# Performance work log

Hardware: AMD Instinct MI355X
Metric: run time of the kernel (lower is better)

The kernel has to match this reference:

```python
import jax, jax.numpy as jnp
import numpy as np

N, E = 100000, 1600000
IN_F, HID, OUT_F, HEADS = 256, 128, 64, 1
C = HID // HEADS  # per-head channels (=128 for heads=1)
NEG_SLOPE = 0.2   # PyG GATConv default leaky_relu slope


def setup_inputs() -> dict:
    key = jax.random.key(0)
    ks = jax.random.split(key, 16)
    w = lambda k, shape, fan: (jax.random.normal(k, shape, jnp.float32) / np.float32(np.sqrt(fan)))
    return {
        "x": jax.random.normal(ks[0], (N, IN_F), jnp.float32),
        "edge_index": jax.random.randint(ks[1], (2, E), 0, N, dtype=jnp.int32),
        "W_in": w(ks[2], (IN_F, HID), IN_F),
        "b_in": jnp.zeros((HID,), jnp.float32),
        "W1": w(ks[3], (HID, HEADS * C), HID),
        "att_src1": w(ks[4], (HEADS, C), C),
        "att_dst1": w(ks[5], (HEADS, C), C),
        "bias1": jnp.zeros((C,), jnp.float32),
        "W2": w(ks[6], (HID, HEADS * C), HID),
        "att_src2": w(ks[7], (HEADS, C), C),
        "att_dst2": w(ks[8], (HEADS, C), C),
        "bias2": jnp.zeros((C,), jnp.float32),
        "W_out": w(ks[9], (HID, OUT_F), HID),
        "b_out": jnp.zeros((OUT_F,), jnp.float32),
    }


def gat_conv(h, src, dst, W, a_src, a_dst, bias):
    """PyG GATConv, concat=False: per-head attention, segment softmax over dst, mean over heads."""
    g = (h @ W).reshape(-1, HEADS, C)                      # [N,H,C]
    alpha_src = jnp.einsum("nhc,hc->nh", g, a_src)         # [N,H]
    alpha_dst = jnp.einsum("nhc,hc->nh", g, a_dst)         # [N,H]
    e = jax.nn.leaky_relu(alpha_src[src] + alpha_dst[dst], NEG_SLOPE)  # [E,H]
    m = jax.ops.segment_max(e, dst, num_segments=N)        # [N,H], -inf for empty segments
    m = jnp.where(jnp.isfinite(m), m, 0.0)
    p = jnp.exp(e - m[dst])
    s = jax.ops.segment_sum(p, dst, num_segments=N)        # [N,H]
    alpha = p / (s[dst] + 1e-16)                           # [E,H]
    msg = g[src] * alpha[..., None]                        # [E,H,C]  (dominant traffic)
    out = jax.ops.segment_sum(msg, dst, num_segments=N)    # [N,H,C]
    return out.mean(axis=1) + bias                         # concat=False -> head average


def reference(x, edge_index, W_in, b_in, W1, att_src1, att_dst1, bias1,
              W2, att_src2, att_dst2, bias2, W_out, b_out):
    src, dst = edge_index[0], edge_index[1]
    h = x @ W_in + b_in
    h = jax.nn.relu(gat_conv(h, src, dst, W1, att_src1, att_dst1, bias1))
    h = jax.nn.relu(gat_conv(h, src, dst, W2, att_src2, att_dst2, bias2))
    return h @ W_out + b_out
```

## Files before the change

### kernel.cpp

```cpp
#include <hip/hip_runtime.h>
#include <hip/hip_fp16.h>
#include <math.h>

#define NN 100000
#define EE 1600000
constexpr int IN_F = 256, HID = 128, OUT_F = 64;

#define NB 196
#define CAP 16384
#define CH 4096
#define NCHUNK 391

#define MAXE 128

typedef __bf16 bf16x8 __attribute__((ext_vector_type(8)));
typedef float  f32x4  __attribute__((ext_vector_type(4)));

__device__ __forceinline__ f32x4 mfma16(bf16x8 a, bf16x8 b, f32x4 c){
  return __builtin_amdgcn_mfma_f32_16x16x32_bf16(a, b, c, 0, 0, 0);
}

__device__ __forceinline__ void fmamix2(float& aLo, float& aHi, __half2 g2, float al){
  asm("v_fma_mix_f32 %0, %2, %3, %0 op_sel:[0,0,0] op_sel_hi:[1,0,0]\n\t"
      "v_fma_mix_f32 %1, %2, %3, %1 op_sel:[1,0,0] op_sel_hi:[1,0,0]"
      : "+v"(aLo), "+v"(aHi) : "v"(g2), "v"(al));
}

__device__ __forceinline__ float wred_max(float v){
#pragma unroll
  for (int m=1; m<64; m<<=1) v = fmaxf(v, __shfl_xor(v, m, 64));
  return v;
}
__device__ __forceinline__ float wred_sum(float v){
#pragma unroll
  for (int m=1; m<64; m<<=1) v += __shfl_xor(v, m, 64);
  return v;
}

__device__ __forceinline__ unsigned fkey(float x){
  unsigned u = __float_as_uint(x);
  return (u & 0x80000000u) ? ~u : (u ^ 0x80000000u);
}
__device__ __forceinline__ float funkey(unsigned k){
  return __uint_as_float((k & 0x80000000u) ? (k ^ 0x80000000u) : ~k);
}

__global__ __launch_bounds__(256) void k_bin(const int* __restrict__ src,
    const int* __restrict__ dst, int* __restrict__ bucketCnt, int* __restrict__ recs)
{
  __shared__ int cnt[NB];
  __shared__ int base[NB];
  const int tid = threadIdx.x;
  const int e0 = blockIdx.x * CH;
  const int ne = min(CH, EE - e0);

  for (int i=tid; i<NB; i+=256) cnt[i] = 0;
  __syncthreads();
  for (int i=tid; i<ne; i+=256) atomicAdd(&cnt[dst[e0+i]>>9], 1);
  __syncthreads();
  for (int i=tid; i<NB; i+=256) base[i] = atomicAdd(&bucketCnt[i], cnt[i]);
  __syncthreads();
  for (int i=tid; i<NB; i+=256) cnt[i] = 0;
  __syncthreads();
  for (int i=tid; i<ne; i+=256){
    int d = dst[e0+i], b = d >> 9;
    int r = atomicAdd(&cnt[b], 1);
    int pos = base[b] + r;
    if (pos < CAP) recs[(size_t)b*CAP + pos] = src[e0+i] | ((d & 511) << 17);
  }
}

__global__ void k_bscan(const int* __restrict__ bucketCnt, int* __restrict__ bucketStart){
  __shared__ int sd[256];
  int t = threadIdx.x;
  int v = (t < NB) ? min(bucketCnt[t], CAP) : 0;
  sd[t] = v; __syncthreads();
#pragma unroll
  for (int off=1; off<256; off<<=1){
    int x = (t >= off) ? sd[t-off] : 0;
    __syncthreads();
    sd[t] += x;
    __syncthreads();
  }
  if (t < NB) bucketStart[t] = sd[t] - v;
}

__global__ __launch_bounds__(512) void k_csr(const int* __restrict__ recs,
    const int* __restrict__ bucketCnt, const int* __restrict__ bucketStart,
    int* __restrict__ rp, int* __restrict__ colsrc)
{
  __shared__ int hist[513];
  __shared__ int srcbuf[CAP];
  const int tid = threadIdx.x;
  const int b = blockIdx.x;
  const int cntb = min(bucketCnt[b], CAP);
  const int bstart = bucketStart[b];
  const int n0 = b << 9;
  const int nnode = min(512, NN - n0);
  const int* rb = recs + (size_t)b*CAP;

  if (tid < 513) hist[tid] = 0;
  if (tid == 511) hist[512] = 0;
  __syncthreads();
  for (int i=tid; i<cntb; i+=512) atomicAdd(&hist[(rb[i] >> 17) + 1], 1);
  __syncthreads();
#pragma unroll
  for (int off=1; off<513; off<<=1){
    int v0 = (tid >= off) ? hist[tid-off] : 0;
    int i1 = tid + 512;
    int v1 = (i1 < 513 && i1 >= off) ? hist[i1-off] : 0;
    __syncthreads();
    hist[tid] += v0;
    if (i1 < 513) hist[i1] += v1;
    __syncthreads();
  }
  for (int l=tid; l<nnode; l+=512) rp[n0+l] = bstart + hist[l];
  if (b == 0 && tid == 0) rp[NN] = EE;
  __syncthreads();
  for (int i=tid; i<cntb; i+=512){
    int rec = rb[i];
    int r = atomicAdd(&hist[rec >> 17], 1);
    srcbuf[r] = rec & 0x1FFFF;
  }
  __syncthreads();
  for (int i=tid; i<cntb; i+=512) colsrc[bstart + i] = srcbuf[i];
}

__global__ void k_wsplit(const float* __restrict__ W, __bf16* __restrict__ hi, __bf16* __restrict__ lo,
                         int K, int N){
  int idx = blockIdx.x*256 + threadIdx.x;
  if (idx >= K*N) return;
  int k = idx / N, n = idx - k*N;
  float v = W[idx];
  __bf16 h = (__bf16)v;
  hi[(size_t)n*K + k] = h;
  lo[(size_t)n*K + k] = (__bf16)(v - (float)h);
}

template<int K, int BN, bool ATT, bool BIAS, bool ASPLIT, int OMODE>
__global__ __launch_bounds__(256, 2) void k_gemm_mfma(
    const float* __restrict__ Af, const __bf16* __restrict__ AhiG, const __bf16* __restrict__ AloG,
    const __bf16* __restrict__ Bhi, const __bf16* __restrict__ Blo,
    const float* __restrict__ bias,
    void* __restrict__ C0, void* __restrict__ C1,
    const float* __restrict__ attS, const float* __restrict__ attD,
    float* __restrict__ asrc, float* __restrict__ adst,
    unsigned* __restrict__ gk, int nrows)
{
  constexpr int NF = BN/16;
  __shared__ __bf16 Ah[256][36];
  __shared__ __bf16 Al[256][36];
  __shared__ __bf16 Bh[BN][36];
  __shared__ __bf16 Bl[BN][36];
  const int tid = threadIdx.x;
  const int w = tid >> 6, lane = tid & 63;
  const int lr = lane & 15, lk = (lane >> 4) * 8;
  const int rowBase = blockIdx.x * 256;

  f32x4 acc[4][NF];
#pragma unroll
  for (int f=0; f<4; f++)
#pragma unroll
    for (int nf=0; nf<NF; nf++) acc[f][nf] = (f32x4)(0.f);

  int agr = rowBase + tid; if (agr >= nrows) agr = nrows - 1;
  const int bn = tid >> 1, bh2 = (tid & 1) * 16;
  const bool bact = tid < BN*2;

  for (int kc=0; kc<K; kc+=32){
    bf16x8 a_h[4], a_l[4];
    if constexpr (ASPLIT){
      const __bf16* ph = AhiG + (size_t)agr*K + kc;
      const __bf16* pl = AloG + (size_t)agr*K + kc;
#pragma unroll
      for (int q=0; q<4; q++){
        a_h[q] = *(const bf16x8*)(ph + q*8);
        a_l[q] = *(const bf16x8*)(pl + q*8);
      }
    } else {
      const float* pa = Af + (size_t)agr*K + kc;
#pragma unroll
      for (int q=0; q<4; q++){
        float4 f0 = *(const float4*)(pa + q*8);
        float4 f1 = *(const float4*)(pa + q*8 + 4);
        float fv[8] = {f0.x,f0.y,f0.z,f0.w, f1.x,f1.y,f1.z,f1.w};
        bf16x8 h8, l8;
#pragma unroll
        for (int u=0; u<8; u++){
          __bf16 h = (__bf16)fv[u];
          h8[u] = h; l8[u] = (__bf16)(fv[u] - (float)h);
        }
        a_h[q] = h8; a_l[q] = l8;
      }
    }
    bf16x8 b_h[2], b_l[2];
    if (bact){
      const __bf16* ph = Bhi + (size_t)bn*K + kc + bh2;
      const __bf16* pl = Blo + (size_t)bn*K + kc + bh2;
      b_h[0] = *(const bf16x8*)ph;  b_h[1] = *(const bf16x8*)(ph + 8);
      b_l[0] = *(const bf16x8*)pl;  b_l[1] = *(const bf16x8*)(pl + 8);
    }
    __syncthreads();
#pragma unroll
    for (int q=0; q<4; q++){
      *(bf16x8*)&Ah[tid][q*8] = a_h[q];
      *(bf16x8*)&Al[tid][q*8] = a_l[q];
    }
    if (bact){
      *(bf16x8*)&Bh[bn][bh2]     = b_h[0];  *(bf16x8*)&Bh[bn][bh2 + 8] = b_h[1];
      *(bf16x8*)&Bl[bn][bh2]     = b_l[0];  *(bf16x8*)&Bl[bn][bh2 + 8] = b_l[1];
    }
    __syncthreads();

    bf16x8 fah[4], fal[4];
#pragma unroll
    for (int f=0; f<4; f++){
      fah[f] = *(const bf16x8*)&Ah[w*64 + f*16 + lr][lk];
      fal[f] = *(const bf16x8*)&Al[w*64 + f*16 + lr][lk];
    }
#pragma unroll
    for (int nf=0; nf<NF; nf++){
      bf16x8 bh = *(const bf16x8*)&Bh[nf*16 + lr][lk];
#pragma unroll
      for (int f=0; f<4; f++) acc[f][nf] = mfma16(fah[f], bh, acc[f][nf]);
#pragma unroll
      for (int f=0; f<4; f++) acc[f][nf] = mfma16(fal[f], bh, acc[f][nf]);
      bf16x8 bl = *(const bf16x8*)&Bl[nf*16 + lr][lk];
#pragma unroll
      for (int f=0; f<4; f++) acc[f][nf] = mfma16(fah[f], bl, acc[f][nf]);
    }
  }

  const int rq = lane >> 4;
  float pmax = -3e38f;
#pragma unroll
  for (int f=0; f<4; f++){
    const int rbase = rowBase + w*64 + f*16 + rq*4;
    if (ATT){
      float ps[4] = {0.f,0.f,0.f,0.f}, pd[4] = {0.f,0.f,0.f,0.f};
#pragma unroll
      for (int nf=0; nf<NF; nf++){
        float sv = attS[nf*16 + lr], dv = attD[nf*16 + lr];
#pragma unroll
        for (int i=0;i<4;i++){
          ps[i] = fmaf(acc[f][nf][i], sv, ps[i]);
          pd[i] = fmaf(acc[f][nf][i], dv, pd[i]);
        }
      }
#pragma unroll
      for (int mm=1; mm<16; mm<<=1){
#pragma unroll
        for (int i=0;i<4;i++){
          ps[i] += __shfl_xor(ps[i], mm, 64);
          pd[i] += __shfl_xor(pd[i], mm, 64);
        }
      }
      if (lr == 0){
#pragma unroll
        for (int i=0;i<4;i++){
          int row = rbase + i;
          if (row < nrows){ asrc[row] = ps[i]; adst[row] = pd[i]; }
        }
        pmax = fmaxf(pmax, fmaxf(fmaxf(ps[0],ps[1]), fmaxf(ps[2],ps[3])));
      }
    }
#pragma unroll
    for (int i=0;i<4;i++){
      int row = rbase + i;
      if (row < nrows){
#pragma unroll
        for (int nf=0; nf<NF; nf++){
          float v = acc[f][nf][i] + (BIAS ? bias[nf*16 + lr] : 0.f);
          size_t cidx = (size_t)row*BN + nf*16 + lr;
          if constexpr (OMODE == 0){
            ((float*)C0)[cidx] = v;
          } else if constexpr (OMODE == 1){
            ((__half*)C0)[cidx] = __float2half(v);
          } else {
            __bf16 h = (__bf16)v;
            ((__bf16*)C0)[cidx] = h;
            ((__bf16*)C1)[cidx] = (__bf16)(v - (float)h);
          }
        }
      }
    }
  }
  if (ATT){
    pmax = wred_max(pmax);
    if (lane == 0) atomicMax(gk, fkey(pmax));
  }
}

__global__ __launch_bounds__(256) void k_agg(const __half* __restrict__ g,
    const float* __restrict__ asrc, const float* __restrict__ adst,
    const int* __restrict__ rp, const int* __restrict__ cs,
    const float* __restrict__ bias, const unsigned* __restrict__ gkey,
    __bf16* __restrict__ outHi, __bf16* __restrict__ outLo)
{
  __shared__ int2 ebuf[4][MAXE];
  int w = threadIdx.x >> 6, lane = threadIdx.x & 63;
  int node = blockIdx.x*4 + w;
  if (node >= NN) return;
  int r0 = rp[node], deg = rp[node+1] - r0;
  float ad = adst[node];
  float tC = funkey(*gkey) + ad;
  float C = (tC > 0.f) ? tC : 0.2f*tC;
  const int eg = lane >> 4, cl = lane & 15;
  const __half* gcl = g + cl*8;

  float ssum = 0.f;
  float a[8] = {0.f,0.f,0.f,0.f,0.f,0.f,0.f,0.f};

  for (int base=0; base<deg; base+=MAXE){
    int cnt = min(deg - base, MAXE);
    int cpad = (cnt + 3) & ~3;
    for (int i = lane; i < cpad; i += 64){
      int sj = 0; float p = 0.f;
      if (i < cnt){
        sj = cs[r0 + base + i];
        float t = asrc[sj] + ad;
        float e = (t > 0.f) ? t : 0.2f*t;
        p = __expf(e - C);
        ssum += p;
      }
      ebuf[w][i] = make_int2(sj, __float_as_int(p));
    }
    int nst = cpad >> 2;
    int2 e0v = ebuf[w][eg];
    float4 g0v = *(const float4*)(gcl + (size_t)e0v.x * HID);
    int2 e1v = e0v; float4 g1v = g0v;
    if (nst > 1){
      e1v = ebuf[w][4 + eg];
      g1v = *(const float4*)(gcl + (size_t)e1v.x * HID);
    }
    for (int j=0; j<nst; ++j){
      float alc = __int_as_float(e0v.y);
      float4 cur = g0v;
      e0v = e1v; g0v = g1v;
      if (j+2 < nst){
        e1v = ebuf[w][4*(j+2) + eg];
        g1v = *(const float4*)(gcl + (size_t)e1v.x * HID);
      }
      const __half2* hp = (const __half2*)&cur;
      fmamix2(a[0], a[1], hp[0], alc);
      fmamix2(a[2], a[3], hp[1], alc);
      fmamix2(a[4], a[5], hp[2], alc);
      fmamix2(a[6], a[7], hp[3], alc);
    }
  }
  ssum = wred_sum(ssum);
#pragma unroll
  for (int u=0;u<8;u++){
    a[u] += __shfl_xor(a[u], 16, 64);
    a[u] += __shfl_xor(a[u], 32, 64);
  }
  if (eg == 0){
    float inv = 1.f/(ssum + 1e-16f);
    bf16x8 hv, lv;
#pragma unroll
    for (int u=0;u<8;u++){
      float o = fmaxf(a[u]*inv + bias[cl*8 + u], 0.f);
      __bf16 h = (__bf16)o;
      hv[u] = h;
      lv[u] = (__bf16)(o - (float)h);
    }
    *(bf16x8*)(outHi + (size_t)node*HID + cl*8) = hv;
    *(bf16x8*)(outLo + (size_t)node*HID + cl*8) = lv;
  }
}

extern "C" void kernel_launch(void* const* d_in, const int* in_sizes, int n_in,
                              void* d_out, int out_size, void* d_ws, size_t ws_size,
                              hipStream_t stream) {
  const float* x     = (const float*)d_in[0];
  const int*   ei    = (const int*)  d_in[1];
  const float* W_in  = (const float*)d_in[2];
  const float* b_in  = (const float*)d_in[3];
  const float* W1    = (const float*)d_in[4];
  const float* as1   = (const float*)d_in[5];
  const float* ad1   = (const float*)d_in[6];
  const float* bias1 = (const float*)d_in[7];
  const float* W2    = (const float*)d_in[8];
  const float* as2   = (const float*)d_in[9];
  const float* ad2   = (const float*)d_in[10];
  const float* bias2 = (const float*)d_in[11];
  const float* W_out = (const float*)d_in[12];
  const float* b_out = (const float*)d_in[13];
  float* out = (float*)d_out;

  char* ws = (char*)d_ws;
  size_t off = 0;
  auto alloc = [&](size_t bytes)->void*{ void* p = ws + off; off += (bytes + 255) & ~255ull; return p; };
  __bf16* Hhi  = (__bf16*)alloc((size_t)NN*HID*2);
  __bf16* Hlo  = (__bf16*)alloc((size_t)NN*HID*2);
  __half* G    = (__half*)alloc((size_t)NN*HID*2);
  __bf16* Ohi  = (__bf16*)alloc((size_t)NN*HID*2);
  __bf16* Olo  = (__bf16*)alloc((size_t)NN*HID*2);
  float*  asrc = (float*) alloc((size_t)NN*4);
  float*  adst = (float*) alloc((size_t)NN*4);
  int*    rp   = (int*)   alloc((size_t)(NN+1)*4);
  int*    colsrc = (int*) alloc((size_t)EE*4);
  int*    recs   = (int*) alloc((size_t)NB*CAP*4);
  int*    bucketCnt   = (int*)alloc(NB*4);
  int*    bucketStart = (int*)alloc(NB*4);
  unsigned* gk1 = (unsigned*)alloc(4);
  unsigned* gk2 = (unsigned*)alloc(4);
  __bf16* whiI = (__bf16*)alloc((size_t)HID*IN_F*2);
  __bf16* wloI = (__bf16*)alloc((size_t)HID*IN_F*2);
  __bf16* whi1 = (__bf16*)alloc((size_t)HID*HID*2);
  __bf16* wlo1 = (__bf16*)alloc((size_t)HID*HID*2);
  __bf16* whi2 = (__bf16*)alloc((size_t)HID*HID*2);
  __bf16* wlo2 = (__bf16*)alloc((size_t)HID*HID*2);
  __bf16* whiO = (__bf16*)alloc((size_t)OUT_F*HID*2);
  __bf16* wloO = (__bf16*)alloc((size_t)OUT_F*HID*2);
  (void)ws_size; (void)in_sizes; (void)n_in; (void)out_size;

  const int* srcIdx = ei;
  const int* dstIdx = ei + EE;

  k_wsplit<<<(IN_F*HID+255)/256, 256, 0, stream>>>(W_in,  whiI, wloI, IN_F, HID);
  k_wsplit<<<(HID*HID+255)/256, 256, 0, stream>>>(W1,    whi1, wlo1, HID, HID);
  k_wsplit<<<(HID*HID+255)/256, 256, 0, stream>>>(W2,    whi2, wlo2, HID, HID);
  k_wsplit<<<(HID*OUT_F+255)/256, 256, 0, stream>>>(W_out, whiO, wloO, HID, OUT_F);

  hipMemsetAsync(bucketCnt, 0, NB*4, stream);
  hipMemsetAsync(gk1, 0, 4, stream);
  hipMemsetAsync(gk2, 0, 4, stream);
  k_bin  <<<NCHUNK, 256, 0, stream>>>(srcIdx, dstIdx, bucketCnt, recs);
  k_bscan<<<1, 256, 0, stream>>>(bucketCnt, bucketStart);
  k_csr  <<<NB, 512, 0, stream>>>(recs, bucketCnt, bucketStart, rp, colsrc);

  const int gblocks = (NN + 255) / 256;
  k_gemm_mfma<256,128,false,true,false,2><<<gblocks, 256, 0, stream>>>(
      x, nullptr, nullptr, whiI, wloI, b_in, Hhi, Hlo, nullptr, nullptr, nullptr, nullptr, nullptr, NN);
  k_gemm_mfma<128,128,true,false,true,1><<<gblocks, 256, 0, stream>>>(
      nullptr, Hhi, Hlo, whi1, wlo1, nullptr, G, nullptr, as1, ad1, asrc, adst, gk1, NN);
  k_agg<<<NN/4, 256, 0, stream>>>(G, asrc, adst, rp, colsrc, bias1, gk1, Ohi, Olo);
  k_gemm_mfma<128,128,true,false,true,1><<<gblocks, 256, 0, stream>>>(
      nullptr, Ohi, Olo, whi2, wlo2, nullptr, G, nullptr, as2, ad2, asrc, adst, gk2, NN);
  k_agg<<<NN/4, 256, 0, stream>>>(G, asrc, adst, rp, colsrc, bias2, gk2, Hhi, Hlo);
  k_gemm_mfma<128,64,false,true,true,0><<<gblocks, 256, 0, stream>>>(
      nullptr, Hhi, Hlo, whiO, wloO, b_out, out, nullptr, nullptr, nullptr, nullptr, nullptr, nullptr, NN);
}
```

Measured before the change: 349.2 us.

## Switch hidden activations to fp16 and split aggregation into alpha and gather kernels

Hidden activations are now stored as single fp16 arrays instead of bf16 hi/lo pairs. The 128-wide GEMMs use f16 MFMA with a scaled hi/lo split of the weights only, which cuts the MFMA count from three to two per tile and halves activation reads and writes. Aggregation is split into a k_alpha kernel that writes normalized (src, alpha) pairs per edge and a k_gather kernel that does the weighted fp16 gather, and the first GEMM gets its own coalesced A loader. This adds an extra 12.8 MB per-edge buffer and an extra launch per layer, and drops the low-order bits of the activations, so accuracy may suffer.

After: 349.9 us. No clear change (+0.2%).

```diff
diff --git a/kernel.cpp b/kernel.cpp
--- a/kernel.cpp
+++ b/kernel.cpp
@@ -11,13 +11,15 @@
 #define CH 4096
 #define NCHUNK 391
 
-#define MAXE 128
-
-typedef __bf16 bf16x8 __attribute__((ext_vector_type(8)));
-typedef float  f32x4  __attribute__((ext_vector_type(4)));
-
-__device__ __forceinline__ f32x4 mfma16(bf16x8 a, bf16x8 b, f32x4 c){
+typedef __bf16    bf16x8 __attribute__((ext_vector_type(8)));
+typedef _Float16  h16x8  __attribute__((ext_vector_type(8)));
+typedef float     f32x4  __attribute__((ext_vector_type(4)));
+
+__device__ __forceinline__ f32x4 mfma16b(bf16x8 a, bf16x8 b, f32x4 c){
   return __builtin_amdgcn_mfma_f32_16x16x32_bf16(a, b, c, 0, 0, 0);
+}
+__device__ __forceinline__ f32x4 mfma16h(h16x8 a, h16x8 b, f32x4 c){
+  return __builtin_amdgcn_mfma_f32_16x16x32_f16(a, b, c, 0, 0, 0);
 }
 
 __device__ __forceinline__ void fmamix2(float& aLo, float& aHi, __half2 g2, float al){
@@ -136,24 +138,123 @@
   hi[(size_t)n*K + k] = h;
   lo[(size_t)n*K + k] = (__bf16)(v - (float)h);
 }
-
-template<int K, int BN, bool ATT, bool BIAS, bool ASPLIT, int OMODE>
-__global__ __launch_bounds__(256, 2) void k_gemm_mfma(
-    const float* __restrict__ Af, const __bf16* __restrict__ AhiG, const __bf16* __restrict__ AloG,
-    const __bf16* __restrict__ Bhi, const __bf16* __restrict__ Blo,
-    const float* __restrict__ bias,
-    void* __restrict__ C0, void* __restrict__ C1,
-    const float* __restrict__ attS, const float* __restrict__ attD,
+__global__ void k_wsplit16(const float* __restrict__ W, _Float16* __restrict__ hi, _Float16* __restrict__ lo,
+                           int K, int N){
+  int idx = blockIdx.x*256 + threadIdx.x;
+  if (idx >= K*N) return;
+  int k = idx / N, n = idx - k*N;
+  float v = W[idx] * 16.f;
+  _Float16 h = (_Float16)v;
+  hi[(size_t)n*K + k] = h;
+  lo[(size_t)n*K + k] = (_Float16)(v - (float)h);
+}
+
+__global__ __launch_bounds__(256, 2) void k_gemm_in(
+    const float* __restrict__ A, const __bf16* __restrict__ Bhi, const __bf16* __restrict__ Blo,
+    const float* __restrict__ bias, __half* __restrict__ C, int nrows)
+{
+  constexpr int K = 256, BN = 128, NF = 8;
+  __shared__ __bf16 Ah[256][36];
+  __shared__ __bf16 Al[256][36];
+  __shared__ __bf16 Bh[BN][36];
+  __shared__ __bf16 Bl[BN][36];
+  const int tid = threadIdx.x, w = tid >> 6, lane = tid & 63;
+  const int lr = lane & 15, lk = (lane >> 4) * 8;
+  const int rowBase = blockIdx.x * 256;
+
+  f32x4 acc[4][NF];
+#pragma unroll
+  for (int f=0; f<4; f++)
+#pragma unroll
+    for (int nf=0; nf<NF; nf++) acc[f][nf] = (f32x4)(0.f);
+
+  const int bn = tid >> 1, bo = (tid & 1) * 16;
+
+  for (int kc=0; kc<K; kc+=32){
+    float4 av[8];
+#pragma unroll
+    for (int k8=0; k8<8; k8++){
+      int P = tid + 256*k8;
+      int r = P >> 3, pc = P & 7;
+      int gr = rowBase + r; if (gr >= nrows) gr = nrows - 1;
+      av[k8] = *(const float4*)(A + (size_t)gr*K + kc + pc*4);
+    }
+    bf16x8 bh0, bh1, bl0, bl1;
+    {
+      const __bf16* ph = Bhi + (size_t)bn*K + kc + bo;
+      const __bf16* pl = Blo + (size_t)bn*K + kc + bo;
+      bh0 = *(const bf16x8*)(ph);  bh1 = *(const bf16x8*)(ph + 8);
+      bl0 = *(const bf16x8*)(pl);  bl1 = *(const bf16x8*)(pl + 8);
+    }
+    __syncthreads();
+#pragma unroll
+    for (int k8=0; k8<8; k8++){
+      int P = tid + 256*k8;
+      int r = P >> 3, pc = P & 7;
+      float fv[4] = {av[k8].x, av[k8].y, av[k8].z, av[k8].w};
+      __bf16 h4[4], l4[4];
+#pragma unroll
+      for (int u=0; u<4; u++){
+        __bf16 h = (__bf16)fv[u];
+        h4[u] = h; l4[u] = (__bf16)(fv[u] - (float)h);
+      }
+      *(uint2*)&Ah[r][pc*4] = *(uint2*)h4;
+      *(uint2*)&Al[r][pc*4] = *(uint2*)l4;
+    }
+    *(bf16x8*)&Bh[bn][bo]     = bh0;  *(bf16x8*)&Bh[bn][bo + 8] = bh1;
+    *(bf16x8*)&Bl[bn][bo]     = bl0;  *(bf16x8*)&Bl[bn][bo + 8] = bl1;
+    __syncthreads();
+
+    bf16x8 fah[4], fal[4];
+#pragma unroll
+    for (int f=0; f<4; f++){
+      fah[f] = *(const bf16x8*)&Ah[w*64 + f*16 + lr][lk];
+      fal[f] = *(const bf16x8*)&Al[w*64 + f*16 + lr][lk];
+    }
+#pragma unroll
+    for (int nf=0; nf<NF; nf++){
+      bf16x8 bh = *(const bf16x8*)&Bh[nf*16 + lr][lk];
+#pragma unroll
+      for (int f=0; f<4; f++) acc[f][nf] = mfma16b(fah[f], bh, acc[f][nf]);
+#pragma unroll
+      for (int f=0; f<4; f++) acc[f][nf] = mfma16b(fal[f], bh, acc[f][nf]);
+      bf16x8 bl = *(const bf16x8*)&Bl[nf*16 + lr][lk];
+#pragma unroll
+      for (int f=0; f<4; f++) acc[f][nf] = mfma16b(fah[f], bl, acc[f][nf]);
+    }
+  }
+
+  const int rq = lane >> 4;
+#pragma unroll
+  for (int f=0; f<4; f++){
+    const int rbase = rowBase + w*64 + f*16 + rq*4;
+#pragma unroll
+    for (int i=0; i<4; i++){
+      int row = rbase + i;
+      if (row < nrows){
+#pragma unroll
+        for (int nf=0; nf<NF; nf++){
+          float v = acc[f][nf][i] + bias[nf*16 + lr];
+          C[(size_t)row*BN + nf*16 + lr] = __float2half(v);
+        }
+      }
+    }
+  }
+}
+
+template<int K, int BN, bool ATT, bool BIAS, int OMODE>
+__global__ __launch_bounds__(256, 2) void k_gemm_f16(
+    const _Float16* __restrict__ A, const _Float16* __restrict__ Whi,
+    const _Float16* __restrict__ Wlo, const float* __restrict__ bias,
+    void* __restrict__ C0, const float* __restrict__ attS, const float* __restrict__ attD,
     float* __restrict__ asrc, float* __restrict__ adst,
     unsigned* __restrict__ gk, int nrows)
 {
   constexpr int NF = BN/16;
-  __shared__ __bf16 Ah[256][36];
-  __shared__ __bf16 Al[256][36];
-  __shared__ __bf16 Bh[BN][36];
-  __shared__ __bf16 Bl[BN][36];
-  const int tid = threadIdx.x;
-  const int w = tid >> 6, lane = tid & 63;
+  __shared__ _Float16 Ah[256][72];
+  __shared__ _Float16 Bh[BN][72];
+  __shared__ _Float16 Bl[BN][72];
+  const int tid = threadIdx.x, w = tid >> 6, lane = tid & 63;
   const int lr = lane & 15, lk = (lane >> 4) * 8;
   const int rowBase = blockIdx.x * 256;
 
@@ -163,73 +264,62 @@
 #pragma unroll
     for (int nf=0; nf<NF; nf++) acc[f][nf] = (f32x4)(0.f);
 
-  int agr = rowBase + tid; if (agr >= nrows) agr = nrows - 1;
-  const int bn = tid >> 1, bh2 = (tid & 1) * 16;
   const bool bact = tid < BN*2;
-
-  for (int kc=0; kc<K; kc+=32){
-    bf16x8 a_h[4], a_l[4];
-    if constexpr (ASPLIT){
-      const __bf16* ph = AhiG + (size_t)agr*K + kc;
-      const __bf16* pl = AloG + (size_t)agr*K + kc;
+  const int bn = tid >> 1, bo = (tid & 1) * 32;
+
+  for (int kc=0; kc<K; kc+=64){
+    h16x8 av[8];
+#pragma unroll
+    for (int k8=0; k8<8; k8++){
+      int P = tid + 256*k8;
+      int r = P >> 3, pc = P & 7;
+      int gr = rowBase + r; if (gr >= nrows) gr = nrows - 1;
+      av[k8] = *(const h16x8*)(A + (size_t)gr*K + kc + pc*8);
+    }
+    h16x8 bhv[4], blv[4];
+    if (bact){
 #pragma unroll
       for (int q=0; q<4; q++){
-        a_h[q] = *(const bf16x8*)(ph + q*8);
-        a_l[q] = *(const bf16x8*)(pl + q*8);
-      }
-    } else {
-      const float* pa = Af + (size_t)agr*K + kc;
+        bhv[q] = *(const h16x8*)(Whi + (size_t)bn*K + kc + bo + q*8);
+        blv[q] = *(const h16x8*)(Wlo + (size_t)bn*K + kc + bo + q*8);
+      }
+    }
+    __syncthreads();
+#pragma unroll
+    for (int k8=0; k8<8; k8++){
+      int P = tid + 256*k8;
+      int r = P >> 3, pc = P & 7;
+      *(h16x8*)&Ah[r][pc*8] = av[k8];
+    }
+    if (bact){
 #pragma unroll
       for (int q=0; q<4; q++){
-        float4 f0 = *(const float4*)(pa + q*8);
-        float4 f1 = *(const float4*)(pa + q*8 + 4);
-        float fv[8] = {f0.x,f0.y,f0.z,f0.w, f1.x,f1.y,f1.z,f1.w};
-        bf16x8 h8, l8;
-#pragma unroll
-        for (int u=0; u<8; u++){
-          __bf16 h = (__bf16)fv[u];
-          h8[u] = h; l8[u] = (__bf16)(fv[u] - (float)h);
-        }
-        a_h[q] = h8; a_l[q] = l8;
-      }
-    }
-    bf16x8 b_h[2], b_l[2];
-    if (bact){
-      const __bf16* ph = Bhi + (size_t)bn*K + kc + bh2;
-      const __bf16* pl = Blo + (size_t)bn*K + kc + bh2;
-      b_h[0] = *(const bf16x8*)ph;  b_h[1] = *(const bf16x8*)(ph + 8);
-      b_l[0] = *(const bf16x8*)pl;  b_l[1] = *(const bf16x8*)(pl + 8);
-    }
-    __syncthreads();
-#pragma unroll
-    for (int q=0; q<4; q++){
-      *(bf16x8*)&Ah[tid][q*8] = a_h[q];
-      *(bf16x8*)&Al[tid][q*8] = a_l[q];
-    }
-    if (bact){
-      *(bf16x8*)&Bh[bn][bh2]     = b_h[0];  *(bf16x8*)&Bh[bn][bh2 + 8] = b_h[1];
-      *(bf16x8*)&Bl[bn][bh2]     = b_l[0];  *(bf16x8*)&Bl[bn][bh2 + 8] = b_l[1];
-    }
-    __syncthreads();
-
-    bf16x8 fah[4], fal[4];
-#pragma unroll
-    for (int f=0; f<4; f++){
-      fah[f] = *(const bf16x8*)&Ah[w*64 + f*16 + lr][lk];
-      fal[f] = *(const bf16x8*)&Al[w*64 + f*16 + lr][lk];
-    }
-#pragma unroll
-    for (int nf=0; nf<NF; nf++){
-      bf16x8 bh = *(const bf16x8*)&Bh[nf*16 + lr][lk];
-#pragma unroll
-      for (int f=0; f<4; f++) acc[f][nf] = mfma16(fah[f], bh, acc[f][nf]);
-#pragma unroll
-      for (int f=0; f<4; f++) acc[f][nf] = mfma16(fal[f], bh, acc[f][nf]);
-      bf16x8 bl = *(const bf16x8*)&Bl[nf*16 + lr][lk];
-#pragma unroll
-      for (int f=0; f<4; f++) acc[f][nf] = mfma16(fah[f], bl, acc[f][nf]);
-    }
-  }
+        *(h16x8*)&Bh[bn][bo + q*8] = bhv[q];
+        *(h16x8*)&Bl[bn][bo + q*8] = blv[q];
+      }
+    }
+    __syncthreads();
+
+#pragma unroll
+    for (int ks=0; ks<64; ks+=32){
+      h16x8 fah[4];
+#pragma unroll
+      for (int f=0; f<4; f++) fah[f] = *(const h16x8*)&Ah[w*64 + f*16 + lr][ks + lk];
+#pragma unroll
+      for (int nf=0; nf<NF; nf++){
+        h16x8 bh = *(const h16x8*)&Bh[nf*16 + lr][ks + lk];
+#pragma unroll
+        for (int f=0; f<4; f++) acc[f][nf] = mfma16h(fah[f], bh, acc[f][nf]);
+        h16x8 bl = *(const h16x8*)&Bl[nf*16 + lr][ks + lk];
+#pragma unroll
+        for (int f=0; f<4; f++) acc[f][nf] = mfma16h(fah[f], bl, acc[f][nf]);
+      }
+    }
+  }
+#pragma unroll
+  for (int f=0; f<4; f++)
+#pragma unroll
+    for (int nf=0; nf<NF; nf++) acc[f][nf] *= 0.0625f;
 
   const int rq = lane >> 4;
   float pmax = -3e38f;
@@ -272,15 +362,8 @@
         for (int nf=0; nf<NF; nf++){
           float v = acc[f][nf][i] + (BIAS ? bias[nf*16 + lr] : 0.f);
           size_t cidx = (size_t)row*BN + nf*16 + lr;
-          if constexpr (OMODE == 0){
-            ((float*)C0)[cidx] = v;
-          } else if constexpr (OMODE == 1){
-            ((__half*)C0)[cidx] = __float2half(v);
-          } else {
-            __bf16 h = (__bf16)v;
-            ((__bf16*)C0)[cidx] = h;
-            ((__bf16*)C1)[cidx] = (__bf16)(v - (float)h);
-          }
+          if constexpr (OMODE == 0) ((float*)C0)[cidx] = v;
+          else                      ((__half*)C0)[cidx] = __float2half(v);
         }
       }
     }
@@ -291,81 +374,107 @@
   }
 }
 
-__global__ __launch_bounds__(256) void k_agg(const __half* __restrict__ g,
+__global__ __launch_bounds__(512) void k_alpha(
     const float* __restrict__ asrc, const float* __restrict__ adst,
     const int* __restrict__ rp, const int* __restrict__ cs,
-    const float* __restrict__ bias, const unsigned* __restrict__ gkey,
-    __bf16* __restrict__ outHi, __bf16* __restrict__ outLo)
+    const unsigned* __restrict__ gkey, int2* __restrict__ epack)
 {
-  __shared__ int2 ebuf[4][MAXE];
   int w = threadIdx.x >> 6, lane = threadIdx.x & 63;
-  int node = blockIdx.x*4 + w;
+  int node = blockIdx.x*8 + w;
   if (node >= NN) return;
   int r0 = rp[node], deg = rp[node+1] - r0;
+  if (deg == 0) return;
   float ad = adst[node];
   float tC = funkey(*gkey) + ad;
   float C = (tC > 0.f) ? tC : 0.2f*tC;
+
+  float p0 = 0.f, p1 = 0.f; int s0 = 0, s1 = 0;
+  float ssum = 0.f;
+  for (int i = lane; i < deg; i += 64){
+    int s = cs[r0 + i];
+    float t = asrc[s] + ad;
+    float e = (t > 0.f) ? t : 0.2f*t;
+    float p = __expf(e - C);
+    ssum += p;
+    if (i < 64)       { p0 = p; s0 = s; }
+    else if (i < 128) { p1 = p; s1 = s; }
+  }
+  ssum = wred_sum(ssum);
+  float inv = 1.f/(ssum + 1e-16f);
+  if (lane < deg)      epack[r0 + lane]      = make_int2(s0, __float_as_int(p0*inv));
+  if (64 + lane < deg) epack[r0 + 64 + lane] = make_int2(s1, __float_as_int(p1*inv));
+  for (int i = 128 + lane; i < deg; i += 64){
+    int s = cs[r0 + i];
+    float t = asrc[s] + ad;
+    float e = (t > 0.f) ? t : 0.2f*t;
+    epack[r0 + i] = make_int2(s, __float_as_int(__expf(e - C)*inv));
+  }
+}
+
+__global__ __launch_bounds__(512) void k_gather(const __half* __restrict__ g,
+    const int2* __restrict__ epack, const int* __restrict__ rp,
+    const float* __restrict__ bias, __half* __restrict__ out)
+{
+  int w = threadIdx.x >> 6, lane = threadIdx.x & 63;
+  int node = blockIdx.x*8 + w;
+  if (node >= NN) return;
+  int r0 = rp[node], deg = rp[node+1] - r0;
   const int eg = lane >> 4, cl = lane & 15;
   const __half* gcl = g + cl*8;
 
-  float ssum = 0.f;
   float a[8] = {0.f,0.f,0.f,0.f,0.f,0.f,0.f,0.f};
-
-  for (int base=0; base<deg; base+=MAXE){
-    int cnt = min(deg - base, MAXE);
-    int cpad = (cnt + 3) & ~3;
-    for (int i = lane; i < cpad; i += 64){
-      int sj = 0; float p = 0.f;
-      if (i < cnt){
-        sj = cs[r0 + base + i];
-        float t = asrc[sj] + ad;
-        float e = (t > 0.f) ? t : 0.2f*t;
-        p = __expf(e - C);
-        ssum += p;
-      }
-      ebuf[w][i] = make_int2(sj, __float_as_int(p));
-    }
-    int nst = cpad >> 2;
-    int2 e0v = ebuf[w][eg];
-    float4 g0v = *(const float4*)(gcl + (size_t)e0v.x * HID);
-    int2 e1v = e0v; float4 g1v = g0v;
-    if (nst > 1){
-      e1v = ebuf[w][4 + eg];
-      g1v = *(const float4*)(gcl + (size_t)e1v.x * HID);
-    }
-    for (int j=0; j<nst; ++j){
-      float alc = __int_as_float(e0v.y);
-      float4 cur = g0v;
-      e0v = e1v; g0v = g1v;
-      if (j+2 < nst){
-        e1v = ebuf[w][4*(j+2) + eg];
-        g1v = *(const float4*)(gcl + (size_t)e1v.x * HID);
+  int nst = (deg + 3) >> 2;
+
+  int2 eA = make_int2(0,0), eB = make_int2(0,0);
+  float4 gA = make_float4(0,0,0,0), gB = make_float4(0,0,0,0);
+  if (nst > 0){
+    if (eg < deg) eA = epack[r0 + eg];
+    gA = *(const float4*)(gcl + (size_t)eA.x * HID);
+  }
+  if (nst > 1){
+    int i1 = 4 + eg;
+    if (i1 < deg) eB = epack[r0 + i1];
+    gB = *(const float4*)(gcl + (size_t)eB.x * HID);
+  }
+  for (int j = 0; j < nst; j += 2){
+    {
+      float al = __int_as_float(eA.y); float4 cur = gA;
+      if (j + 2 < nst){
+        int ii = 4*(j+2) + eg;
+        eA = (ii < deg) ? epack[r0 + ii] : make_int2(0,0);
+        gA = *(const float4*)(gcl + (size_t)eA.x * HID);
       }
       const __half2* hp = (const __half2*)&cur;
-      fmamix2(a[0], a[1], hp[0], alc);
-      fmamix2(a[2], a[3], hp[1], alc);
-      fmamix2(a[4], a[5], hp[2], alc);
-      fmamix2(a[6], a[7], hp[3], alc);
-    }
-  }
-  ssum = wred_sum(ssum);
-#pragma unroll
-  for (int u=0;u<8;u++){
+      fmamix2(a[0], a[1], hp[0], al);
+      fmamix2(a[2], a[3], hp[1], al);
+      fmamix2(a[4], a[5], hp[2], al);
+      fmamix2(a[6], a[7], hp[3], al);
+    }
+    if (j + 1 < nst){
+      float al = __int_as_float(eB.y); float4 cur = gB;
+      if (j + 3 < nst){
+        int ii = 4*(j+3) + eg;
+        eB = (ii < deg) ? epack[r0 + ii] : make_int2(0,0);
+        gB = *(const float4*)(gcl + (size_t)eB.x * HID);
+      }
+      const __half2* hp = (const __half2*)&cur;
+      fmamix2(a[0], a[1], hp[0], al);
+      fmamix2(a[2], a[3], hp[1], al);
+      fmamix2(a[4], a[5], hp[2], al);
+      fmamix2(a[6], a[7], hp[3], al);
+    }
+  }
+#pragma unroll
+  for (int u=0; u<8; u++){
     a[u] += __shfl_xor(a[u], 16, 64);
     a[u] += __shfl_xor(a[u], 32, 64);
   }
   if (eg == 0){
-    float inv = 1.f/(ssum + 1e-16f);
-    bf16x8 hv, lv;
-#pragma unroll
-    for (int u=0;u<8;u++){
-      float o = fmaxf(a[u]*inv + bias[cl*8 + u], 0.f);
-      __bf16 h = (__bf16)o;
-      hv[u] = h;
-      lv[u] = (__bf16)(o - (float)h);
-    }
-    *(bf16x8*)(outHi + (size_t)node*HID + cl*8) = hv;
-    *(bf16x8*)(outLo + (size_t)node*HID + cl*8) = lv;
+    __half hv[8];
+#pragma unroll
+    for (int u=0; u<8; u++)
+      hv[u] = __float2half(fmaxf(a[u] + bias[cl*8 + u], 0.f));
+    *(float4*)(out + (size_t)node*HID + cl*8) = *(float4*)hv;
   }
 }
 
@@ -391,37 +500,36 @@
   char* ws = (char*)d_ws;
   size_t off = 0;
   auto alloc = [&](size_t bytes)->void*{ void* p = ws + off; off += (bytes + 255) & ~255ull; return p; };
-  __bf16* Hhi  = (__bf16*)alloc((size_t)NN*HID*2);
-  __bf16* Hlo  = (__bf16*)alloc((size_t)NN*HID*2);
-  __half* G    = (__half*)alloc((size_t)NN*HID*2);
-  __bf16* Ohi  = (__bf16*)alloc((size_t)NN*HID*2);
-  __bf16* Olo  = (__bf16*)alloc((size_t)NN*HID*2);
-  float*  asrc = (float*) alloc((size_t)NN*4);
-  float*  adst = (float*) alloc((size_t)NN*4);
-  int*    rp   = (int*)   alloc((size_t)(NN+1)*4);
-  int*    colsrc = (int*) alloc((size_t)EE*4);
-  int*    recs   = (int*) alloc((size_t)NB*CAP*4);
-  int*    bucketCnt   = (int*)alloc(NB*4);
-  int*    bucketStart = (int*)alloc(NB*4);
+  __half*   H    = (__half*)  alloc((size_t)NN*HID*2);
+  __half*   G    = (__half*)  alloc((size_t)NN*HID*2);
+  __half*   O1   = (__half*)  alloc((size_t)NN*HID*2);
+  float*    asrc = (float*)   alloc((size_t)NN*4);
+  float*    adst = (float*)   alloc((size_t)NN*4);
+  int*      rp   = (int*)     alloc((size_t)(NN+1)*4);
+  int*      colsrc = (int*)   alloc((size_t)EE*4);
+  int2*     epack  = (int2*)  alloc((size_t)EE*8);
+  int*      recs   = (int*)   alloc((size_t)NB*CAP*4);
+  int*      bucketCnt   = (int*)alloc(NB*4);
+  int*      bucketStart = (int*)alloc(NB*4);
   unsigned* gk1 = (unsigned*)alloc(4);
   unsigned* gk2 = (unsigned*)alloc(4);
-  __bf16* whiI = (__bf16*)alloc((size_t)HID*IN_F*2);
-  __bf16* wloI = (__bf16*)alloc((size_t)HID*IN_F*2);
-  __bf16* whi1 = (__bf16*)alloc((size_t)HID*HID*2);
-  __bf16* wlo1 = (__bf16*)alloc((size_t)HID*HID*2);
-  __bf16* whi2 = (__bf16*)alloc((size_t)HID*HID*2);
-  __bf16* wlo2 = (__bf16*)alloc((size_t)HID*HID*2);
-  __bf16* whiO = (__bf16*)alloc((size_t)OUT_F*HID*2);
-  __bf16* wloO = (__bf16*)alloc((size_t)OUT_F*HID*2);
+  __bf16*   whiI = (__bf16*) alloc((size_t)HID*IN_F*2);
+  __bf16*   wloI = (__bf16*) alloc((size_t)HID*IN_F*2);
+  _Float16* w1h  = (_Float16*)alloc((size_t)HID*HID*2);
+  _Float16* w1l  = (_Float16*)alloc((size_t)HID*HID*2);
+  _Float16* w2h  = (_Float16*)alloc((size_t)HID*HID*2);
+  _Float16* w2l  = (_Float16*)alloc((size_t)HID*HID*2);
+  _Float16* wOh  = (_Float16*)alloc((size_t)OUT_F*HID*2);
+  _Float16* wOl  = (_Float16*)alloc((size_t)OUT_F*HID*2);
   (void)ws_size; (void)in_sizes; (void)n_in; (void)out_size;
 
   const int* srcIdx = ei;
   const int* dstIdx = ei + EE;
 
-  k_wsplit<<<(IN_F*HID+255)/256, 256, 0, stream>>>(W_in,  whiI, wloI, IN_F, HID);
-  k_wsplit<<<(HID*HID+255)/256, 256, 0, stream>>>(W1,    whi1, wlo1, HID, HID);
-  k_wsplit<<<(HID*HID+255)/256, 256, 0, stream>>>(W2,    whi2, wlo2, HID, HID);
-  k_wsplit<<<(HID*OUT_F+255)/256, 256, 0, stream>>>(W_out, whiO, wloO, HID, OUT_F);
+  k_wsplit  <<<(IN_F*HID+255)/256, 256, 0, stream>>>(W_in,  whiI, wloI, IN_F, HID);
+  k_wsplit16<<<(HID*HID+255)/256, 256, 0, stream>>>(W1,    w1h, w1l, HID, HID);
+  k_wsplit16<<<(HID*HID+255)/256, 256, 0, stream>>>(W2,    w2h, w2l, HID, HID);
+  k_wsplit16<<<(HID*OUT_F+255)/256, 256, 0, stream>>>(W_out, wOh, wOl, HID, OUT_F);
 
   hipMemsetAsync(bucketCnt, 0, NB*4, stream);
   hipMemsetAsync(gk1, 0, 4, stream);
@@ -431,14 +539,16 @@
   k_csr  <<<NB, 512, 0, stream>>>(recs, bucketCnt, bucketStart, rp, colsrc);
 
   const int gblocks = (NN + 255) / 256;
-  k_gemm_mfma<256,128,false,true,false,2><<<gblocks, 256, 0, stream>>>(
-      x, nullptr, nullptr, whiI, wloI, b_in, Hhi, Hlo, nullptr, nullptr, nullptr, nullptr, nullptr, NN);
-  k_gemm_mfma<128,128,true,false,true,1><<<gblocks, 256, 0, stream>>>(
-      nullptr, Hhi, Hlo, whi1, wlo1, nullptr, G, nullptr, as1, ad1, asrc, adst, gk1, NN);
-  k_agg<<<NN/4, 256, 0, stream>>>(G, asrc, adst, rp, colsrc, bias1, gk1, Ohi, Olo);
-  k_gemm_mfma<128,128,true,false,true,1><<<gblocks, 256, 0, stream>>>(
-      nullptr, Ohi, Olo, whi2, wlo2, nullptr, G, nullptr, as2, ad2, asrc, adst, gk2, NN);
-  k_agg<<<NN/4, 256, 0, stream>>>(G, asrc, adst, rp, colsrc, bias2, gk2, Hhi, Hlo);
-  k_gemm_mfma<128,64,false,true,true,0><<<gblocks, 256, 0, stream>>>(
-      nullptr, Hhi, Hlo, whiO, wloO, b_out, out, nullptr, nullptr, nullptr, nullptr, nullptr, nullptr, NN);
-}
+  const int ablocks = (NN + 7) / 8;
+  k_gemm_in<<<gblocks, 256, 0, stream>>>(x, whiI, wloI, b_in, H, NN);
+  k_gemm_f16<128,128,true,false,1><<<gblocks, 256, 0, stream>>>(
+      (const _Float16*)H, w1h, w1l, nullptr, G, as1, ad1, asrc, adst, gk1, NN);
+  k_alpha <<<ablocks, 512, 0, stream>>>(asrc, adst, rp, colsrc, gk1, epack);
+  k_gather<<<ablocks, 512, 0, stream>>>(G, epack, rp, bias1, O1);
+  k_gemm_f16<128,128,true,false,1><<<gblocks, 256, 0, stream>>>(
+      (const _Float16*)O1, w2h, w2l, nullptr, G, as2, ad2, asrc, adst, gk2, NN);
+  k_alpha <<<ablocks, 512, 0, stream>>>(asrc, adst, rp, colsrc, gk2, epack);
+  k_gather<<<ablocks, 512, 0, stream>>>(G, epack, rp, bias2, (__half*)H);
+  k_gemm_f16<128,64,false,true,0><<<gblocks, 256, 0, stream>>>(
+      (const _Float16*)H, wOh, wOl, b_out, out, nullptr, nullptr, nullptr, nullptr, nullptr, NN);
+}
```
